# Performance work log

Hardware: AMD Instinct MI355X
Metric: run time of the kernel (lower is better)

## Reference

```python
import jax, jax.numpy as jnp
import numpy as np

E, K = 8, 2            # num_experts, top_k
H, F = 1024, 1024      # hidden_size, ffn_hidden_size
T = 2048               # tokens (batch*seq)


def setup_inputs() -> dict:
    key = jax.random.key(0)
    k1, k2, k3, k4 = jax.random.split(key, 4)
    x = jax.random.normal(k1, (T, H), jnp.float32)
    gate_w = jax.random.normal(k2, (E, H), jnp.float32) * 0.02   # router FastLinear weight [E, H]
    w1_v1 = jax.random.normal(k3, (E, 2 * F, H), jnp.float32) * 0.02  # cat([w1, v1], dim=0) per expert
    w2 = jax.random.normal(k4, (E, H, F), jnp.float32) * 0.02    # down-proj FastLinear weight [H, F]
    return {"x": x, "gate_w": gate_w, "w1_v1": w1_v1, "w2": w2}


def reference(x, gate_w, w1_v1, w2):
    # Router: logits -> softmax -> top-k gating weights (DBRX style)
    logits = x @ gate_w.T                       # [T, E]
    probs = jax.nn.softmax(logits, axis=-1)
    top_w, top_e = jax.lax.top_k(probs, K)      # [T, K]
    # Dense combine matrix [T, E]: gating weight if expert selected, else 0
    combine = jnp.zeros((x.shape[0], E), x.dtype).at[
        jnp.arange(x.shape[0])[:, None], top_e
    ].add(top_w)
    # Per-expert GLU MLP, batched over experts (grouped GEMM equivalent)
    gv = jnp.einsum('th,efh->etf', x, w1_v1)    # [E, T, 2F]
    g, v = jnp.split(gv, 2, axis=-1)            # each [E, T, F]
    hidden = jax.nn.silu(g) * v                 # [E, T, F]
    outs = jnp.einsum('etf,ehf->eth', hidden, w2)  # [E, T, H]
    # Combine: weighted sum over selected experts
    return jnp.einsum('eth,te->th', outs, combine)  # [T, H]
```

## Files before the change

### kernel.cpp

```cpp
#include <hip/hip_runtime.h>
#include <hip/hip_bf16.h>

#define T_TOK 2048
#define HID   1024
#define FF    1024
#define NE    8
#define CNT_STRIDE 64
#define RBLK 8

using short8   = __attribute__((ext_vector_type(8))) short;
using f32x4    = __attribute__((ext_vector_type(4))) float;

__device__ __forceinline__ unsigned short f32_to_bf16(float f) {
  union { float f; unsigned int u; } v; v.f = f;
  unsigned int r = v.u + 0x7fffu + ((v.u >> 16) & 1u);
  return (unsigned short)(r >> 16);
}

__device__ __forceinline__ void gload_lds16(const unsigned short* g, unsigned short* l) {
  __builtin_amdgcn_global_load_lds(
      (const __attribute__((address_space(1))) void*)g,
      (__attribute__((address_space(3))) void*)l, 16, 0, 0);
}

__global__ __launch_bounds__(256) void convertw_kernel(const float* __restrict__ s1,
                                                       const float* __restrict__ s2,
                                                       unsigned short* __restrict__ d1,
                                                       unsigned short* __restrict__ d2,
                                                       int n1_4, int ntot_4) {
  int i = blockIdx.x * 256 + threadIdx.x;
  if (i >= ntot_4) return;
  const float* s; unsigned short* d; int k;
  if (i < n1_4) { s = s1; d = d1; k = i; }
  else          { s = s2; d = d2; k = i - n1_4; }
  const float4 v = ((const float4*)s)[k];
  ushort4 o;
  o.x = f32_to_bf16(v.x); o.y = f32_to_bf16(v.y);
  o.z = f32_to_bf16(v.z); o.w = f32_to_bf16(v.w);
  ((ushort4*)d)[k] = o;
}

__global__ __launch_bounds__(256) void router_kernel(const float* __restrict__ x,
                                                     const float* __restrict__ gw,
                                                     int* __restrict__ counts,
                                                     int* __restrict__ toks,
                                                     float* __restrict__ wts,
                                                     unsigned short* __restrict__ xb) {
  __shared__ float gws[NE * HID];
  __shared__ int   s_e[RBLK * 2];
  __shared__ float s_w[RBLK * 2];
  int tid = threadIdx.x;
  int lane = tid & 63, wid = tid >> 6;
  int t0 = blockIdx.x * RBLK;

  float4 greg[8];
#pragma unroll
  for (int j = 0; j < 8; ++j) greg[j] = ((const float4*)gw)[j * 256 + tid];

  float4 xv[2][4];
#pragma unroll
  for (int tk = 0; tk < 2; ++tk) {
    const float4* xr4 = (const float4*)(x + (size_t)(t0 + wid * 2 + tk) * HID);
#pragma unroll
    for (int c = 0; c < 4; ++c) xv[tk][c] = xr4[c * 64 + lane];
  }

#pragma unroll
  for (int j = 0; j < 8; ++j) ((float4*)&gws[0])[j * 256 + tid] = greg[j];
  __syncthreads();

#pragma unroll
  for (int tk = 0; tk < 2; ++tk) {
    unsigned short* xrow = xb + (size_t)(t0 + wid * 2 + tk) * HID;
#pragma unroll
    for (int c = 0; c < 4; ++c) {
      ushort4 o;
      o.x = f32_to_bf16(xv[tk][c].x); o.y = f32_to_bf16(xv[tk][c].y);
      o.z = f32_to_bf16(xv[tk][c].z); o.w = f32_to_bf16(xv[tk][c].w);
      *(ushort4*)&xrow[(c * 64 + lane) * 4] = o;
    }
  }

  float acc[2][NE];
#pragma unroll
  for (int tk = 0; tk < 2; ++tk)
#pragma unroll
    for (int e = 0; e < NE; ++e) acc[tk][e] = 0.f;

#pragma unroll
  for (int c = 0; c < 4; ++c) {
#pragma unroll
    for (int e = 0; e < NE; ++e) {
      const float4 gv = *(const float4*)&gws[e * HID + (c * 64 + lane) * 4];
#pragma unroll
      for (int tk = 0; tk < 2; ++tk) {
        acc[tk][e] = fmaf(xv[tk][c].x, gv.x, acc[tk][e]);
        acc[tk][e] = fmaf(xv[tk][c].y, gv.y, acc[tk][e]);
        acc[tk][e] = fmaf(xv[tk][c].z, gv.z, acc[tk][e]);
        acc[tk][e] = fmaf(xv[tk][c].w, gv.w, acc[tk][e]);
      }
    }
  }

#pragma unroll
  for (int tk = 0; tk < 2; ++tk) {
#pragma unroll
    for (int off = 32; off >= 1; off >>= 1) {
#pragma unroll
      for (int e = 0; e < NE; ++e) acc[tk][e] += __shfl_xor(acc[tk][e], off);
    }
    if (lane == 0) {
      int local = wid * 2 + tk;
      float m = acc[tk][0];
#pragma unroll
      for (int e = 1; e < NE; ++e) m = fmaxf(m, acc[tk][e]);
      float p[NE], s = 0.f;
#pragma unroll
      for (int e = 0; e < NE; ++e) { p[e] = __expf(acc[tk][e] - m); s += p[e]; }
      float inv = 1.f / s;

      int e1 = 0; float b1 = p[0];
#pragma unroll
      for (int e = 1; e < NE; ++e) if (p[e] > b1) { b1 = p[e]; e1 = e; }
      int e2 = -1; float b2 = -1.f;
#pragma unroll
      for (int e = 0; e < NE; ++e) if (e != e1 && p[e] > b2) { b2 = p[e]; e2 = e; }

      s_e[local * 2]     = e1;  s_w[local * 2]     = b1 * inv;
      s_e[local * 2 + 1] = e2;  s_w[local * 2 + 1] = b2 * inv;
    }
  }
  __syncthreads();

  if (tid < NE) {
    int c = 0;
#pragma unroll
    for (int i = 0; i < RBLK * 2; ++i) c += (s_e[i] == tid);
    if (c > 0) {
      int base = atomicAdd(&counts[tid * CNT_STRIDE], c);
      int p = 0;
      for (int i = 0; i < RBLK * 2; ++i) {
        if (s_e[i] == tid) {
          toks[tid * T_TOK + base + p] = t0 + (i >> 1);
          wts[tid * T_TOK + base + p] = s_w[i];
          ++p;
        }
      }
    }
  }
}

__global__ __launch_bounds__(256) void gemm1_kernel(const unsigned short* __restrict__ xb,
                                                    const unsigned short* __restrict__ w1b,
                                                    const int* __restrict__ counts,
                                                    const int* __restrict__ toks,
                                                    unsigned short* __restrict__ hidden) {
  int e = blockIdx.z;
  int cnt = counts[e * CNT_STRIDE];
  int m0 = blockIdx.y * 128;
  if (m0 >= cnt) return;
  int n0 = blockIdx.x * 64;
  const unsigned short* W = w1b + (size_t)e * (2 * FF * HID);

  __shared__ unsigned short sA[128 * 64];
  __shared__ unsigned short sBg[64 * 64];
  __shared__ unsigned short sBv[64 * 64];

  int tid = threadIdx.x;
  int lane = tid & 63, wid = tid >> 6;

  const unsigned short* aptr[4]; int adst[4];
#pragma unroll
  for (int j = 0; j < 4; ++j) {
    int q = tid + 256 * j;
    int row = q >> 3, u = q & 7;
    int gr = m0 + row;
    int tok = (gr < cnt) ? toks[e * T_TOK + gr] : 0;
    int su = u ^ (row & 7);
    aptr[j] = xb + (size_t)tok * HID + su * 8;
    adst[j] = q * 8;
  }
  const unsigned short* bgptr[2]; const unsigned short* bvptr[2]; int bdst[2];
#pragma unroll
  for (int j = 0; j < 2; ++j) {
    int q = tid + 256 * j;
    int row = q >> 3, u = q & 7;
    int su = u ^ (row & 7);
    bgptr[j] = W + (size_t)(n0 + row) * HID + su * 8;
    bvptr[j] = W + (size_t)(FF + n0 + row) * HID + su * 8;
    bdst[j] = q * 8;
  }

  f32x4 accg[2][4], accv[2][4];
#pragma unroll
  for (int m = 0; m < 2; ++m)
#pragma unroll
    for (int n = 0; n < 4; ++n) {
      accg[m][n] = (f32x4){0.f, 0.f, 0.f, 0.f};
      accv[m][n] = (f32x4){0.f, 0.f, 0.f, 0.f};
    }

  for (int k0 = 0; k0 < HID; k0 += 64) {
#pragma unroll
    for (int j = 0; j < 4; ++j) gload_lds16(aptr[j] + k0, &sA[adst[j]]);
#pragma unroll
    for (int j = 0; j < 2; ++j) {
      gload_lds16(bgptr[j] + k0, &sBg[bdst[j]]);
      gload_lds16(bvptr[j] + k0, &sBv[bdst[j]]);
    }
    __syncthreads();
#pragma unroll
    for (int kk = 0; kk < 2; ++kk) {
      short8 af[2], bgf[4], bvf[4];
#pragma unroll
      for (int m = 0; m < 2; ++m) {
        int row = wid * 32 + m * 16 + (lane & 15);
        int u = (kk * 4 + (lane >> 4)) ^ (row & 7);
        af[m] = *(const short8*)&sA[row * 64 + u * 8];
      }
#pragma unroll
      for (int n = 0; n < 4; ++n) {
        int row = n * 16 + (lane & 15);
        int u = (kk * 4 + (lane >> 4)) ^ (row & 7);
        bgf[n] = *(const short8*)&sBg[row * 64 + u * 8];
        bvf[n] = *(const short8*)&sBv[row * 64 + u * 8];
      }
#pragma unroll
      for (int m = 0; m < 2; ++m)
#pragma unroll
        for (int n = 0; n < 4; ++n) {
          accg[m][n] = __builtin_amdgcn_mfma_f32_16x16x32_bf16(af[m], bgf[n], accg[m][n], 0, 0, 0);
          accv[m][n] = __builtin_amdgcn_mfma_f32_16x16x32_bf16(af[m], bvf[n], accv[m][n], 0, 0, 0);
        }
    }
    __syncthreads();
  }

  unsigned short* Hseg = hidden + (size_t)e * T_TOK * FF;
#pragma unroll
  for (int m = 0; m < 2; ++m) {
#pragma unroll
    for (int j = 0; j < 4; ++j) {
      int row = wid * 32 + m * 16 + (lane >> 4) * 4 + j;
      int gr = m0 + row;
      if (gr < cnt) {
#pragma unroll
        for (int n = 0; n < 4; ++n) {
          int col = n0 + n * 16 + (lane & 15);
          float g = accg[m][n][j];
          float v = accv[m][n][j];
          float val = (g / (1.f + __expf(-g))) * v;
          Hseg[(size_t)gr * FF + col] = f32_to_bf16(val);
        }
      }
    }
  }
}

__global__ __launch_bounds__(256) void gemm2_kernel(const unsigned short* __restrict__ hidden,
                                                    const unsigned short* __restrict__ w2b,
                                                    const int* __restrict__ counts,
                                                    const int* __restrict__ toks,
                                                    const float* __restrict__ wts,
                                                    float* __restrict__ out) {
  int e = blockIdx.z;
  int cnt = counts[e * CNT_STRIDE];
  int m0 = blockIdx.y * 128;
  if (m0 >= cnt) return;
  int n0 = blockIdx.x * 64;
  const unsigned short* A = hidden + (size_t)e * T_TOK * FF;
  const unsigned short* W = w2b + (size_t)e * HID * FF;

  __shared__ unsigned short sA[128 * 64];
  __shared__ unsigned short sB[64 * 64];

  int tid = threadIdx.x;
  int lane = tid & 63, wid = tid >> 6;

  const unsigned short* aptr[4]; int adst[4];
#pragma unroll
  for (int j = 0; j < 4; ++j) {
    int q = tid + 256 * j;
    int row = q >> 3, u = q & 7;
    int su = u ^ (row & 7);
    aptr[j] = A + (size_t)(m0 + row) * FF + su * 8;
    adst[j] = q * 8;
  }
  const unsigned short* bptr[2]; int bdst[2];
#pragma unroll
  for (int j = 0; j < 2; ++j) {
    int q = tid + 256 * j;
    int row = q >> 3, u = q & 7;
    int su = u ^ (row & 7);
    bptr[j] = W + (size_t)(n0 + row) * FF + su * 8;
    bdst[j] = q * 8;
  }

  f32x4 acc[2][4];
#pragma unroll
  for (int m = 0; m < 2; ++m)
#pragma unroll
    for (int n = 0; n < 4; ++n) acc[m][n] = (f32x4){0.f, 0.f, 0.f, 0.f};

  for (int k0 = 0; k0 < FF; k0 += 64) {
#pragma unroll
    for (int j = 0; j < 4; ++j) gload_lds16(aptr[j] + k0, &sA[adst[j]]);
#pragma unroll
    for (int j = 0; j < 2; ++j) gload_lds16(bptr[j] + k0, &sB[bdst[j]]);
    __syncthreads();
#pragma unroll
    for (int kk = 0; kk < 2; ++kk) {
      short8 af[2], bf[4];
#pragma unroll
      for (int m = 0; m < 2; ++m) {
        int row = wid * 32 + m * 16 + (lane & 15);
        int u = (kk * 4 + (lane >> 4)) ^ (row & 7);
        af[m] = *(const short8*)&sA[row * 64 + u * 8];
      }
#pragma unroll
      for (int n = 0; n < 4; ++n) {
        int row = n * 16 + (lane & 15);
        int u = (kk * 4 + (lane >> 4)) ^ (row & 7);
        bf[n] = *(const short8*)&sB[row * 64 + u * 8];
      }
#pragma unroll
      for (int m = 0; m < 2; ++m)
#pragma unroll
        for (int n = 0; n < 4; ++n)
          acc[m][n] = __builtin_amdgcn_mfma_f32_16x16x32_bf16(af[m], bf[n], acc[m][n], 0, 0, 0);
    }
    __syncthreads();
  }

#pragma unroll
  for (int m = 0; m < 2; ++m) {
#pragma unroll
    for (int j = 0; j < 4; ++j) {
      int row = wid * 32 + m * 16 + (lane >> 4) * 4 + j;
      int gr = m0 + row;
      if (gr < cnt) {
        int tok = toks[e * T_TOK + gr];
        float wt = wts[e * T_TOK + gr];
#pragma unroll
        for (int n = 0; n < 4; ++n) {
          int col = n0 + n * 16 + (lane & 15);
          atomicAdd(&out[(size_t)tok * HID + col], acc[m][n][j] * wt);
        }
      }
    }
  }
}

extern "C" void kernel_launch(void* const* d_in, const int* in_sizes, int n_in,
                              void* d_out, int out_size, void* d_ws, size_t ws_size,
                              hipStream_t stream) {
  const float* x  = (const float*)d_in[0];
  const float* gw = (const float*)d_in[1];
  const float* w1 = (const float*)d_in[2];
  const float* w2 = (const float*)d_in[3];
  float* out = (float*)d_out;

  char* ws = (char*)d_ws;
  int*   counts = (int*)ws;
  int*   toks   = (int*)(ws + 4096);
  float* wts    = (float*)(ws + 4096 + 65536);
  unsigned short* xb  = (unsigned short*)(ws + 135168);
  unsigned short* w1b = xb + (size_t)T_TOK * HID;
  unsigned short* w2b = w1b + (size_t)NE * 2 * FF * HID;
  unsigned short* hid = w2b + (size_t)NE * HID * FF;

  hipMemsetAsync(counts, 0, 4096, stream);
  hipMemsetAsync(d_out, 0, (size_t)out_size * sizeof(float), stream);

  router_kernel<<<T_TOK / RBLK, 256, 0, stream>>>(x, gw, counts, toks, wts, xb);

  const int n1_4 = NE * 2 * FF * HID / 4;
  const int ntot_4 = n1_4 + NE * HID * FF / 4;
  convertw_kernel<<<(ntot_4 + 255) / 256, 256, 0, stream>>>(w1, w2, w1b, w2b, n1_4, ntot_4);

  gemm1_kernel<<<dim3(FF / 64, T_TOK / 128, NE), 256, 0, stream>>>(xb, w1b, counts, toks, hid);
  gemm2_kernel<<<dim3(HID / 64, T_TOK / 128, NE), 256, 0, stream>>>(hid, w2b, counts, toks, wts, out);
}
```

Baseline: 207.9 us.

## Double-buffer LDS tiles in both expert GEMM kernels to overlap loads with MFMA

Both grouped GEMM kernels now keep two LDS buffers per operand. The next K-tile is prefetched with global_load_lds while MFMAs run on the current tile. This aims to hide global memory latency that was previously exposed by the load-then-barrier pattern. It doubles LDS usage per block, which may reduce occupancy, and relies on the end-of-iteration barrier to wait for the in-flight loads.

```diff
diff --git a/kernel.cpp b/kernel.cpp
--- a/kernel.cpp
+++ b/kernel.cpp
@@ -162,9 +162,9 @@
   int n0 = blockIdx.x * 64;
   const unsigned short* W = w1b + (size_t)e * (2 * FF * HID);
 
-  __shared__ unsigned short sA[128 * 64];
-  __shared__ unsigned short sBg[64 * 64];
-  __shared__ unsigned short sBv[64 * 64];
+  __shared__ unsigned short sA[2][128 * 64];
+  __shared__ unsigned short sBg[2][64 * 64];
+  __shared__ unsigned short sBv[2][64 * 64];
 
   int tid = threadIdx.x;
   int lane = tid & 63, wid = tid >> 6;
@@ -200,15 +200,28 @@
       accv[m][n] = (f32x4){0.f, 0.f, 0.f, 0.f};
     }
 
-  for (int k0 = 0; k0 < HID; k0 += 64) {
-#pragma unroll
-    for (int j = 0; j < 4; ++j) gload_lds16(aptr[j] + k0, &sA[adst[j]]);
-#pragma unroll
-    for (int j = 0; j < 2; ++j) {
-      gload_lds16(bgptr[j] + k0, &sBg[bdst[j]]);
-      gload_lds16(bvptr[j] + k0, &sBv[bdst[j]]);
-    }
-    __syncthreads();
+#pragma unroll
+  for (int j = 0; j < 4; ++j) gload_lds16(aptr[j], &sA[0][adst[j]]);
+#pragma unroll
+  for (int j = 0; j < 2; ++j) {
+    gload_lds16(bgptr[j], &sBg[0][bdst[j]]);
+    gload_lds16(bvptr[j], &sBv[0][bdst[j]]);
+  }
+  __syncthreads();
+
+  for (int t = 0; t < HID / 64; ++t) {
+    int cur = t & 1;
+    if (t < HID / 64 - 1) {
+      int k0n = (t + 1) * 64;
+      int nxt = cur ^ 1;
+#pragma unroll
+      for (int j = 0; j < 4; ++j) gload_lds16(aptr[j] + k0n, &sA[nxt][adst[j]]);
+#pragma unroll
+      for (int j = 0; j < 2; ++j) {
+        gload_lds16(bgptr[j] + k0n, &sBg[nxt][bdst[j]]);
+        gload_lds16(bvptr[j] + k0n, &sBv[nxt][bdst[j]]);
+      }
+    }
 #pragma unroll
     for (int kk = 0; kk < 2; ++kk) {
       short8 af[2], bgf[4], bvf[4];
@@ -216,14 +229,14 @@
       for (int m = 0; m < 2; ++m) {
         int row = wid * 32 + m * 16 + (lane & 15);
         int u = (kk * 4 + (lane >> 4)) ^ (row & 7);
-        af[m] = *(const short8*)&sA[row * 64 + u * 8];
+        af[m] = *(const short8*)&sA[cur][row * 64 + u * 8];
       }
 #pragma unroll
       for (int n = 0; n < 4; ++n) {
         int row = n * 16 + (lane & 15);
         int u = (kk * 4 + (lane >> 4)) ^ (row & 7);
-        bgf[n] = *(const short8*)&sBg[row * 64 + u * 8];
-        bvf[n] = *(const short8*)&sBv[row * 64 + u * 8];
+        bgf[n] = *(const short8*)&sBg[cur][row * 64 + u * 8];
+        bvf[n] = *(const short8*)&sBv[cur][row * 64 + u * 8];
       }
 #pragma unroll
       for (int m = 0; m < 2; ++m)
@@ -271,8 +284,8 @@
   const unsigned short* A = hidden + (size_t)e * T_TOK * FF;
   const unsigned short* W = w2b + (size_t)e * HID * FF;
 
-  __shared__ unsigned short sA[128 * 64];
-  __shared__ unsigned short sB[64 * 64];
+  __shared__ unsigned short sA[2][128 * 64];
+  __shared__ unsigned short sB[2][64 * 64];
 
   int tid = threadIdx.x;
   int lane = tid & 63, wid = tid >> 6;
@@ -302,12 +315,22 @@
 #pragma unroll
     for (int n = 0; n < 4; ++n) acc[m][n] = (f32x4){0.f, 0.f, 0.f, 0.f};
 
-  for (int k0 = 0; k0 < FF; k0 += 64) {
-#pragma unroll
-    for (int j = 0; j < 4; ++j) gload_lds16(aptr[j] + k0, &sA[adst[j]]);
-#pragma unroll
-    for (int j = 0; j < 2; ++j) gload_lds16(bptr[j] + k0, &sB[bdst[j]]);
-    __syncthreads();
+#pragma unroll
+  for (int j = 0; j < 4; ++j) gload_lds16(aptr[j], &sA[0][adst[j]]);
+#pragma unroll
+  for (int j = 0; j < 2; ++j) gload_lds16(bptr[j], &sB[0][bdst[j]]);
+  __syncthreads();
+
+  for (int t = 0; t < FF / 64; ++t) {
+    int cur = t & 1;
+    if (t < FF / 64 - 1) {
+      int k0n = (t + 1) * 64;
+      int nxt = cur ^ 1;
+#pragma unroll
+      for (int j = 0; j < 4; ++j) gload_lds16(aptr[j] + k0n, &sA[nxt][adst[j]]);
+#pragma unroll
+      for (int j = 0; j < 2; ++j) gload_lds16(bptr[j] + k0n, &sB[nxt][bdst[j]]);
+    }
 #pragma unroll
     for (int kk = 0; kk < 2; ++kk) {
       short8 af[2], bf[4];
@@ -315,13 +338,13 @@
       for (int m = 0; m < 2; ++m) {
         int row = wid * 32 + m * 16 + (lane & 15);
         int u = (kk * 4 + (lane >> 4)) ^ (row & 7);
-        af[m] = *(const short8*)&sA[row * 64 + u * 8];
+        af[m] = *(const short8*)&sA[cur][row * 64 + u * 8];
       }
 #pragma unroll
       for (int n = 0; n < 4; ++n) {
         int row = n * 16 + (lane & 15);
         int u = (kk * 4 + (lane >> 4)) ^ (row & 7);
-        bf[n] = *(const short8*)&sB[row * 64 + u * 8];
+        bf[n] = *(const short8*)&sB[cur][row * 64 + u * 8];
       }
 #pragma unroll
       for (int m = 0; m < 2; ++m)
```

After: 218.4 us. +5.0%, slower.

## Fuse fp32-to-bf16 weight conversion into GEMM tile loads

Applied to the files above, without the earlier changes.

Removes the separate weight conversion kernel and its bf16 workspace copies. Each GEMM block now loads fp32 weights through registers, converts them to bf16 and stores them to LDS. This avoids a full pass over all expert weights, but replaces asynchronous direct-to-LDS loads with synchronous register loads and re-reads fp32 weights once per m-block.

```diff
diff --git a/kernel.cpp b/kernel.cpp
--- a/kernel.cpp
+++ b/kernel.cpp
@@ -16,28 +16,18 @@
   unsigned int r = v.u + 0x7fffu + ((v.u >> 16) & 1u);
   return (unsigned short)(r >> 16);
 }
+__device__ __forceinline__ unsigned int pack2(float a, float b) {
+  return (unsigned int)f32_to_bf16(a) | ((unsigned int)f32_to_bf16(b) << 16);
+}
+__device__ __forceinline__ uint4 pack8(const float4 lo, const float4 hi) {
+  return make_uint4(pack2(lo.x, lo.y), pack2(lo.z, lo.w),
+                    pack2(hi.x, hi.y), pack2(hi.z, hi.w));
+}
 
 __device__ __forceinline__ void gload_lds16(const unsigned short* g, unsigned short* l) {
   __builtin_amdgcn_global_load_lds(
       (const __attribute__((address_space(1))) void*)g,
       (__attribute__((address_space(3))) void*)l, 16, 0, 0);
-}
-
-__global__ __launch_bounds__(256) void convertw_kernel(const float* __restrict__ s1,
-                                                       const float* __restrict__ s2,
-                                                       unsigned short* __restrict__ d1,
-                                                       unsigned short* __restrict__ d2,
-                                                       int n1_4, int ntot_4) {
-  int i = blockIdx.x * 256 + threadIdx.x;
-  if (i >= ntot_4) return;
-  const float* s; unsigned short* d; int k;
-  if (i < n1_4) { s = s1; d = d1; k = i; }
-  else          { s = s2; d = d2; k = i - n1_4; }
-  const float4 v = ((const float4*)s)[k];
-  ushort4 o;
-  o.x = f32_to_bf16(v.x); o.y = f32_to_bf16(v.y);
-  o.z = f32_to_bf16(v.z); o.w = f32_to_bf16(v.w);
-  ((ushort4*)d)[k] = o;
 }
 
 __global__ __launch_bounds__(256) void router_kernel(const float* __restrict__ x,
@@ -151,7 +141,7 @@
 }
 
 __global__ __launch_bounds__(256) void gemm1_kernel(const unsigned short* __restrict__ xb,
-                                                    const unsigned short* __restrict__ w1b,
+                                                    const float* __restrict__ w1f,
                                                     const int* __restrict__ counts,
                                                     const int* __restrict__ toks,
                                                     unsigned short* __restrict__ hidden) {
@@ -160,7 +150,7 @@
   int m0 = blockIdx.y * 128;
   if (m0 >= cnt) return;
   int n0 = blockIdx.x * 64;
-  const unsigned short* W = w1b + (size_t)e * (2 * FF * HID);
+  const float* Wf = w1f + (size_t)e * (2 * FF * HID);
 
   __shared__ unsigned short sA[128 * 64];
   __shared__ unsigned short sBg[64 * 64];
@@ -180,14 +170,14 @@
     aptr[j] = xb + (size_t)tok * HID + su * 8;
     adst[j] = q * 8;
   }
-  const unsigned short* bgptr[2]; const unsigned short* bvptr[2]; int bdst[2];
+  const float* bgp[2]; const float* bvp[2]; int bdst[2];
 #pragma unroll
   for (int j = 0; j < 2; ++j) {
     int q = tid + 256 * j;
     int row = q >> 3, u = q & 7;
     int su = u ^ (row & 7);
-    bgptr[j] = W + (size_t)(n0 + row) * HID + su * 8;
-    bvptr[j] = W + (size_t)(FF + n0 + row) * HID + su * 8;
+    bgp[j] = Wf + (size_t)(n0 + row) * HID + su * 8;
+    bvp[j] = Wf + (size_t)(FF + n0 + row) * HID + su * 8;
     bdst[j] = q * 8;
   }
 
@@ -205,8 +195,12 @@
     for (int j = 0; j < 4; ++j) gload_lds16(aptr[j] + k0, &sA[adst[j]]);
 #pragma unroll
     for (int j = 0; j < 2; ++j) {
-      gload_lds16(bgptr[j] + k0, &sBg[bdst[j]]);
-      gload_lds16(bvptr[j] + k0, &sBv[bdst[j]]);
+      float4 g0 = *(const float4*)(bgp[j] + k0);
+      float4 g1 = *(const float4*)(bgp[j] + k0 + 4);
+      float4 v0 = *(const float4*)(bvp[j] + k0);
+      float4 v1 = *(const float4*)(bvp[j] + k0 + 4);
+      *(uint4*)&sBg[bdst[j]] = pack8(g0, g1);
+      *(uint4*)&sBv[bdst[j]] = pack8(v0, v1);
     }
     __syncthreads();
 #pragma unroll
@@ -258,7 +252,7 @@
 }
 
 __global__ __launch_bounds__(256) void gemm2_kernel(const unsigned short* __restrict__ hidden,
-                                                    const unsigned short* __restrict__ w2b,
+                                                    const float* __restrict__ w2f,
                                                     const int* __restrict__ counts,
                                                     const int* __restrict__ toks,
                                                     const float* __restrict__ wts,
@@ -269,7 +263,7 @@
   if (m0 >= cnt) return;
   int n0 = blockIdx.x * 64;
   const unsigned short* A = hidden + (size_t)e * T_TOK * FF;
-  const unsigned short* W = w2b + (size_t)e * HID * FF;
+  const float* Wf = w2f + (size_t)e * HID * FF;
 
   __shared__ unsigned short sA[128 * 64];
   __shared__ unsigned short sB[64 * 64];
@@ -286,13 +280,13 @@
     aptr[j] = A + (size_t)(m0 + row) * FF + su * 8;
     adst[j] = q * 8;
   }
-  const unsigned short* bptr[2]; int bdst[2];
+  const float* bp[2]; int bdst[2];
 #pragma unroll
   for (int j = 0; j < 2; ++j) {
     int q = tid + 256 * j;
     int row = q >> 3, u = q & 7;
     int su = u ^ (row & 7);
-    bptr[j] = W + (size_t)(n0 + row) * FF + su * 8;
+    bp[j] = Wf + (size_t)(n0 + row) * FF + su * 8;
     bdst[j] = q * 8;
   }
 
@@ -306,7 +300,11 @@
 #pragma unroll
     for (int j = 0; j < 4; ++j) gload_lds16(aptr[j] + k0, &sA[adst[j]]);
 #pragma unroll
-    for (int j = 0; j < 2; ++j) gload_lds16(bptr[j] + k0, &sB[bdst[j]]);
+    for (int j = 0; j < 2; ++j) {
+      float4 b0 = *(const float4*)(bp[j] + k0);
+      float4 b1 = *(const float4*)(bp[j] + k0 + 4);
+      *(uint4*)&sB[bdst[j]] = pack8(b0, b1);
+    }
     __syncthreads();
 #pragma unroll
     for (int kk = 0; kk < 2; ++kk) {
@@ -365,19 +363,13 @@
   int*   toks   = (int*)(ws + 4096);
   float* wts    = (float*)(ws + 4096 + 65536);
   unsigned short* xb  = (unsigned short*)(ws + 135168);
-  unsigned short* w1b = xb + (size_t)T_TOK * HID;
-  unsigned short* w2b = w1b + (size_t)NE * 2 * FF * HID;
-  unsigned short* hid = w2b + (size_t)NE * HID * FF;
+  unsigned short* hid = xb + (size_t)T_TOK * HID;
 
   hipMemsetAsync(counts, 0, 4096, stream);
   hipMemsetAsync(d_out, 0, (size_t)out_size * sizeof(float), stream);
 
   router_kernel<<<T_TOK / RBLK, 256, 0, stream>>>(x, gw, counts, toks, wts, xb);
 
-  const int n1_4 = NE * 2 * FF * HID / 4;
-  const int ntot_4 = n1_4 + NE * HID * FF / 4;
-  convertw_kernel<<<(ntot_4 + 255) / 256, 256, 0, stream>>>(w1, w2, w1b, w2b, n1_4, ntot_4);
-
-  gemm1_kernel<<<dim3(FF / 64, T_TOK / 128, NE), 256, 0, stream>>>(xb, w1b, counts, toks, hid);
-  gemm2_kernel<<<dim3(HID / 64, T_TOK / 128, NE), 256, 0, stream>>>(hid, w2b, counts, toks, wts, out);
-}
+  gemm1_kernel<<<dim3(FF / 64, T_TOK / 128, NE), 256, 0, stream>>>(xb, w1, counts, toks, hid);
+  gemm2_kernel<<<dim3(HID / 64, T_TOK / 128, NE), 256, 0, stream>>>(hid, w2, counts, toks, wts, out);
+}
```

New measurement: 224.1 us. 7.8% more time.

## Double-buffer LDS tiles with prefetch in both expert GEMM kernels

Applied to the files above, without the earlier changes.

Both grouped GEMM kernels switch from a single 64-wide K tile to two 32-wide LDS buffers. The next tile is issued via global-to-LDS loads while the current one is consumed by MFMA. The XOR swizzle is adapted to four 16-byte chunks per row. The aim is to hide global load latency behind compute, at the cost of more loop iterations and barriers per K.

```diff
diff --git a/kernel.cpp b/kernel.cpp
--- a/kernel.cpp
+++ b/kernel.cpp
@@ -162,33 +162,32 @@
   int n0 = blockIdx.x * 64;
   const unsigned short* W = w1b + (size_t)e * (2 * FF * HID);
 
-  __shared__ unsigned short sA[128 * 64];
-  __shared__ unsigned short sBg[64 * 64];
-  __shared__ unsigned short sBv[64 * 64];
+  __shared__ unsigned short sA[2][128 * 32];
+  __shared__ unsigned short sBg[2][64 * 32];
+  __shared__ unsigned short sBv[2][64 * 32];
 
   int tid = threadIdx.x;
   int lane = tid & 63, wid = tid >> 6;
 
-  const unsigned short* aptr[4]; int adst[4];
-#pragma unroll
-  for (int j = 0; j < 4; ++j) {
+  const unsigned short* aptr[2]; int adst[2];
+#pragma unroll
+  for (int j = 0; j < 2; ++j) {
     int q = tid + 256 * j;
-    int row = q >> 3, u = q & 7;
+    int row = q >> 2, u = q & 3;
     int gr = m0 + row;
     int tok = (gr < cnt) ? toks[e * T_TOK + gr] : 0;
-    int su = u ^ (row & 7);
+    int su = u ^ ((row >> 1) & 3);
     aptr[j] = xb + (size_t)tok * HID + su * 8;
     adst[j] = q * 8;
   }
-  const unsigned short* bgptr[2]; const unsigned short* bvptr[2]; int bdst[2];
-#pragma unroll
-  for (int j = 0; j < 2; ++j) {
-    int q = tid + 256 * j;
-    int row = q >> 3, u = q & 7;
-    int su = u ^ (row & 7);
-    bgptr[j] = W + (size_t)(n0 + row) * HID + su * 8;
-    bvptr[j] = W + (size_t)(FF + n0 + row) * HID + su * 8;
-    bdst[j] = q * 8;
+  const unsigned short* bgptr; const unsigned short* bvptr; int bdst;
+  {
+    int q = tid;
+    int row = q >> 2, u = q & 3;
+    int su = u ^ ((row >> 1) & 3);
+    bgptr = W + (size_t)(n0 + row) * HID + su * 8;
+    bvptr = W + (size_t)(FF + n0 + row) * HID + su * 8;
+    bdst = q * 8;
   }
 
   f32x4 accg[2][4], accv[2][4];
@@ -200,30 +199,37 @@
       accv[m][n] = (f32x4){0.f, 0.f, 0.f, 0.f};
     }
 
-  for (int k0 = 0; k0 < HID; k0 += 64) {
-#pragma unroll
-    for (int j = 0; j < 4; ++j) gload_lds16(aptr[j] + k0, &sA[adst[j]]);
-#pragma unroll
-    for (int j = 0; j < 2; ++j) {
-      gload_lds16(bgptr[j] + k0, &sBg[bdst[j]]);
-      gload_lds16(bvptr[j] + k0, &sBv[bdst[j]]);
-    }
-    __syncthreads();
-#pragma unroll
-    for (int kk = 0; kk < 2; ++kk) {
+#pragma unroll
+  for (int j = 0; j < 2; ++j) gload_lds16(aptr[j], &sA[0][adst[j]]);
+  gload_lds16(bgptr, &sBg[0][bdst]);
+  gload_lds16(bvptr, &sBv[0][bdst]);
+  __syncthreads();
+
+  const int NT = HID / 32;
+  for (int t = 0; t < NT; ++t) {
+    int cur = t & 1;
+    if (t < NT - 1) {
+      int k0n = (t + 1) * 32;
+      int nxt = cur ^ 1;
+#pragma unroll
+      for (int j = 0; j < 2; ++j) gload_lds16(aptr[j] + k0n, &sA[nxt][adst[j]]);
+      gload_lds16(bgptr + k0n, &sBg[nxt][bdst]);
+      gload_lds16(bvptr + k0n, &sBv[nxt][bdst]);
+    }
+    {
       short8 af[2], bgf[4], bvf[4];
 #pragma unroll
       for (int m = 0; m < 2; ++m) {
         int row = wid * 32 + m * 16 + (lane & 15);
-        int u = (kk * 4 + (lane >> 4)) ^ (row & 7);
-        af[m] = *(const short8*)&sA[row * 64 + u * 8];
+        int u = (lane >> 4) ^ ((row >> 1) & 3);
+        af[m] = *(const short8*)&sA[cur][row * 32 + u * 8];
       }
 #pragma unroll
       for (int n = 0; n < 4; ++n) {
         int row = n * 16 + (lane & 15);
-        int u = (kk * 4 + (lane >> 4)) ^ (row & 7);
-        bgf[n] = *(const short8*)&sBg[row * 64 + u * 8];
-        bvf[n] = *(const short8*)&sBv[row * 64 + u * 8];
+        int u = (lane >> 4) ^ ((row >> 1) & 3);
+        bgf[n] = *(const short8*)&sBg[cur][row * 32 + u * 8];
+        bvf[n] = *(const short8*)&sBv[cur][row * 32 + u * 8];
       }
 #pragma unroll
       for (int m = 0; m < 2; ++m)
@@ -271,29 +277,28 @@
   const unsigned short* A = hidden + (size_t)e * T_TOK * FF;
   const unsigned short* W = w2b + (size_t)e * HID * FF;
 
-  __shared__ unsigned short sA[128 * 64];
-  __shared__ unsigned short sB[64 * 64];
+  __shared__ unsigned short sA[2][128 * 32];
+  __shared__ unsigned short sB[2][64 * 32];
 
   int tid = threadIdx.x;
   int lane = tid & 63, wid = tid >> 6;
 
-  const unsigned short* aptr[4]; int adst[4];
-#pragma unroll
-  for (int j = 0; j < 4; ++j) {
+  const unsigned short* aptr[2]; int adst[2];
+#pragma unroll
+  for (int j = 0; j < 2; ++j) {
     int q = tid + 256 * j;
-    int row = q >> 3, u = q & 7;
-    int su = u ^ (row & 7);
+    int row = q >> 2, u = q & 3;
+    int su = u ^ ((row >> 1) & 3);
     aptr[j] = A + (size_t)(m0 + row) * FF + su * 8;
     adst[j] = q * 8;
   }
-  const unsigned short* bptr[2]; int bdst[2];
-#pragma unroll
-  for (int j = 0; j < 2; ++j) {
-    int q = tid + 256 * j;
-    int row = q >> 3, u = q & 7;
-    int su = u ^ (row & 7);
-    bptr[j] = W + (size_t)(n0 + row) * FF + su * 8;
-    bdst[j] = q * 8;
+  const unsigned short* bptr; int bdst;
+  {
+    int q = tid;
+    int row = q >> 2, u = q & 3;
+    int su = u ^ ((row >> 1) & 3);
+    bptr = W + (size_t)(n0 + row) * FF + su * 8;
+    bdst = q * 8;
   }
 
   f32x4 acc[2][4];
@@ -302,26 +307,34 @@
 #pragma unroll
     for (int n = 0; n < 4; ++n) acc[m][n] = (f32x4){0.f, 0.f, 0.f, 0.f};
 
-  for (int k0 = 0; k0 < FF; k0 += 64) {
-#pragma unroll
-    for (int j = 0; j < 4; ++j) gload_lds16(aptr[j] + k0, &sA[adst[j]]);
-#pragma unroll
-    for (int j = 0; j < 2; ++j) gload_lds16(bptr[j] + k0, &sB[bdst[j]]);
-    __syncthreads();
-#pragma unroll
-    for (int kk = 0; kk < 2; ++kk) {
+#pragma unroll
+  for (int j = 0; j < 2; ++j) gload_lds16(aptr[j], &sA[0][adst[j]]);
+  gload_lds16(bptr, &sB[0][bdst]);
+  __syncthreads();
+
+  const int NT = FF / 32;
+  for (int t = 0; t < NT; ++t) {
+    int cur = t & 1;
+    if (t < NT - 1) {
+      int k0n = (t + 1) * 32;
+      int nxt = cur ^ 1;
+#pragma unroll
+      for (int j = 0; j < 2; ++j) gload_lds16(aptr[j] + k0n, &sA[nxt][adst[j]]);
+      gload_lds16(bptr + k0n, &sB[nxt][bdst]);
+    }
+    {
       short8 af[2], bf[4];
 #pragma unroll
       for (int m = 0; m < 2; ++m) {
         int row = wid * 32 + m * 16 + (lane & 15);
-        int u = (kk * 4 + (lane >> 4)) ^ (row & 7);
-        af[m] = *(const short8*)&sA[row * 64 + u * 8];
+        int u = (lane >> 4) ^ ((row >> 1) & 3);
+        af[m] = *(const short8*)&sA[cur][row * 32 + u * 8];
       }
 #pragma unroll
       for (int n = 0; n < 4; ++n) {
         int row = n * 16 + (lane & 15);
-        int u = (kk * 4 + (lane >> 4)) ^ (row & 7);
-        bf[n] = *(const short8*)&sB[row * 64 + u * 8];
+        int u = (lane >> 4) ^ ((row >> 1) & 3);
+        bf[n] = *(const short8*)&sB[cur][row * 32 + u * 8];
       }
 #pragma unroll
       for (int m = 0; m < 2; ++m)
```

Result: slower. 225.1 us (+8.3%).
